# Optimization experiments

Hardware: AMD Instinct MI355X
Metric: run time of the kernel (lower is better)

The kernel has to match this reference:

```python
import math
import jax, jax.numpy as jnp
import numpy as np

BSZ, SEQ, DIM = 2, 2048, 4096
N_HEADS, N_KV = 32, 8
HEAD_DIM = DIM // N_HEADS  # 128
N_REP = N_HEADS // N_KV    # 4
EPS = 1e-5
ROPE_THETA = 500000.0


def setup_inputs() -> dict:
    key = jax.random.key(0)
    ks = jax.random.split(key, 6)
    scale = 0.02
    x = jax.random.normal(ks[0], (BSZ, SEQ, DIM), dtype=jnp.float32)
    wq = jax.random.normal(ks[1], (N_HEADS * HEAD_DIM, DIM), dtype=jnp.float32) * scale
    wk = jax.random.normal(ks[2], (N_KV * HEAD_DIM, DIM), dtype=jnp.float32) * scale
    wv = jax.random.normal(ks[3], (N_KV * HEAD_DIM, DIM), dtype=jnp.float32) * scale
    wo = jax.random.normal(ks[4], (N_HEADS * HEAD_DIM, DIM), dtype=jnp.float32).T * scale  # [DIM, n_heads*hd] -> stored as [out,in]
    wo = jax.random.normal(ks[4], (DIM, N_HEADS * HEAD_DIM), dtype=jnp.float32) * scale
    # RoPE tables (real/imag parts of freqs_cis)
    inv_freq = 1.0 / (ROPE_THETA ** (jnp.arange(0, HEAD_DIM, 2, dtype=jnp.float32) / HEAD_DIM))
    angles = jnp.arange(SEQ, dtype=jnp.float32)[:, None] * inv_freq[None, :]  # [SEQ, HEAD_DIM//2]
    cos, sin = jnp.cos(angles), jnp.sin(angles)
    # causal additive mask
    neg_inf = jnp.finfo(jnp.float32).min
    mask = jnp.where(jnp.tril(jnp.ones((SEQ, SEQ), dtype=bool)), 0.0, neg_inf).astype(jnp.float32)
    return {"x": x, "wq": wq, "wk": wk, "wv": wv, "wo": wo,
            "cos": cos, "sin": sin, "mask": mask, "start_pos": 0}


def _apply_rope(t, cos, sin):
    # t: [b, s, h, hd]; pairs (even, odd) as in view_as_complex
    tf = t.astype(jnp.float32).reshape(*t.shape[:-1], HEAD_DIM // 2, 2)
    e, o = tf[..., 0], tf[..., 1]
    c = cos[None, :, None, :]
    s = sin[None, :, None, :]
    out = jnp.stack([e * c - o * s, e * s + o * c], axis=-1)
    return out.reshape(t.shape).astype(t.dtype)


def _rmsnorm(t):
    tf = t.astype(jnp.float32)
    return (tf * jax.lax.rsqrt(jnp.mean(tf * tf, axis=-1, keepdims=True) + EPS)).astype(t.dtype)


def reference(x, wq, wk, wv, wo, cos, sin, mask, start_pos):
    b, s, _ = x.shape
    xq = (x @ wq.T).reshape(b, s, N_HEADS, HEAD_DIM)
    xk = (x @ wk.T).reshape(b, s, N_KV, HEAD_DIM)
    xv = (x @ wv.T).reshape(b, s, N_KV, HEAD_DIM)
    xq = _apply_rope(xq, cos, sin)
    xk = _apply_rope(xk, cos, sin)
    xq = _rmsnorm(xq)
    xk = _rmsnorm(xk)
    # KV cache write/read with start_pos=0 over seqlen tokens is identity here.
    # GQA without repeat_interleave: q head h attends kv head h // N_REP
    q = xq.transpose(0, 2, 1, 3).reshape(b, N_KV, N_REP, s, HEAD_DIM)
    k = xk.transpose(0, 2, 1, 3)  # [b, n_kv, s, hd]
    v = xv.transpose(0, 2, 1, 3)
    scale = 1.0 / math.sqrt(HEAD_DIM)
    scores = jnp.einsum('bgrqd,bgkd->bgrqk', q, k) * scale + mask[None, None, None]
    probs = jax.nn.softmax(scores, axis=-1)
    out = jnp.einsum('bgrqk,bgkd->bgrqd', probs, v)
    out = out.reshape(b, N_HEADS, s, HEAD_DIM).transpose(0, 2, 1, 3).reshape(b, s, N_HEADS * HEAD_DIM)
    return out @ wo.T
```

## Files before the change

kernel.cpp:

```cpp
#include <hip/hip_runtime.h>
#include <hip/hip_bf16.h>
#include <stdint.h>

#define SEQ 2048
#define DIMSZ 4096
#define QKVN 6144

typedef __attribute__((ext_vector_type(8))) __bf16 bf16x8;
typedef __attribute__((ext_vector_type(4))) float f32x4;

static __device__ __forceinline__ void gld_lds16(const void* g, void* l) {
  __builtin_amdgcn_global_load_lds(
      (__attribute__((address_space(1))) void*)(g),
      (__attribute__((address_space(3))) void*)(l), 16, 0, 0);
}

__global__ __launch_bounds__(256) void k_cvt5(const float* __restrict__ x,
                                              const float* __restrict__ wq,
                                              const float* __restrict__ wk,
                                              const float* __restrict__ wv,
                                              const float* __restrict__ wo,
                                              __bf16* __restrict__ xb,
                                              __bf16* __restrict__ wqkvb,
                                              __bf16* __restrict__ wob) {
  long vid = (long)blockIdx.x * 256 + threadIdx.x;
  const long stride = (long)gridDim.x * 256;
  for (; vid < 7340032L; vid += stride) {
    const float* src; __bf16* dst; long off;
    if (vid < 2097152L)      { src = x;  dst = xb;                off = vid; }
    else if (vid < 4194304L) { src = wq; dst = wqkvb;             off = vid - 2097152L; }
    else if (vid < 4718592L) { src = wk; dst = wqkvb + 16777216L; off = vid - 4194304L; }
    else if (vid < 5242880L) { src = wv; dst = wqkvb + 20971520L; off = vid - 4718592L; }
    else                     { src = wo; dst = wob;               off = vid - 5242880L; }
    const long e = off * 8;
    float4 v0 = *(const float4*)(src + e);
    float4 v1 = *(const float4*)(src + e + 4);
    bf16x8 o;
    o[0] = (__bf16)v0.x; o[1] = (__bf16)v0.y; o[2] = (__bf16)v0.z; o[3] = (__bf16)v0.w;
    o[4] = (__bf16)v1.x; o[5] = (__bf16)v1.y; o[6] = (__bf16)v1.z; o[7] = (__bf16)v1.w;
    *(bf16x8*)(dst + e) = o;
  }
}

template <typename OutT>
__global__ __launch_bounds__(512) void k_gemm8p(const __bf16* __restrict__ A,
                                                const __bf16* __restrict__ B,
                                                OutT* __restrict__ C,
                                                int M, int N, int K) {
  __shared__ __align__(16) __bf16 As[2][2][128 * 64];
  __shared__ __align__(16) __bf16 Bs[2][2][128 * 64];
  const int t = threadIdx.x;
  const int l = t & 63;
  const int w = t >> 6;
  const int wm = w >> 2;
  const int wn = w & 3;
  const int lr = l & 15, lg = l >> 4;
  const int sw = lr & 7;
  const int bm = blockIdx.y, bn = blockIdx.x;

  const int srow = t >> 3;
  const int scol = ((t & 7) ^ (srow & 7)) << 3;
  const __bf16* pa0 = A + (size_t)(bm * 256 +   0 + srow) * K + scol;
  const __bf16* pa1 = A + (size_t)(bm * 256 +  64 + srow) * K + scol;
  const __bf16* pa2 = A + (size_t)(bm * 256 + 128 + srow) * K + scol;
  const __bf16* pa3 = A + (size_t)(bm * 256 + 192 + srow) * K + scol;
  const __bf16* pb0 = B + (size_t)(bn * 256 +   0 + srow) * K + scol;
  const __bf16* pb1 = B + (size_t)(bn * 256 +  64 + srow) * K + scol;
  const __bf16* pb2 = B + (size_t)(bn * 256 + 128 + srow) * K + scol;
  const __bf16* pb3 = B + (size_t)(bn * 256 + 192 + srow) * K + scol;
  const int ldst = t * 8;

#define SA0(buf, kc) { gld_lds16(pa0 + (kc), &As[buf][0][ldst]); gld_lds16(pa1 + (kc), &As[buf][0][4096 + ldst]); }
#define SA1(buf, kc) { gld_lds16(pa2 + (kc), &As[buf][1][ldst]); gld_lds16(pa3 + (kc), &As[buf][1][4096 + ldst]); }
#define SB0(buf, kc) { gld_lds16(pb0 + (kc), &Bs[buf][0][ldst]); gld_lds16(pb1 + (kc), &Bs[buf][0][4096 + ldst]); }
#define SB1(buf, kc) { gld_lds16(pb2 + (kc), &Bs[buf][1][ldst]); gld_lds16(pb3 + (kc), &Bs[buf][1][4096 + ldst]); }

  const int c0 = ((lg ^ sw) * 8);
  const int c1 = (((lg ^ sw) ^ 4) * 8);
  const int aRow = lr;
  const int bRow = (wn & 1) * 64 + lr;

#define RDA(mi0, cur)                                                          \
  _Pragma("unroll") for (int mi = 0; mi < 4; ++mi) {                           \
    a[mi][0] = *(const bf16x8*)&As[cur][wm][(((mi0) + mi) * 16 + aRow) * 64 + c0]; \
    a[mi][1] = *(const bf16x8*)&As[cur][wm][(((mi0) + mi) * 16 + aRow) * 64 + c1]; \
  }
#define RDB(bv, ni0, cur)                                                      \
  _Pragma("unroll") for (int ni = 0; ni < 2; ++ni) {                           \
    bv[ni][0] = *(const bf16x8*)&Bs[cur][wn >> 1][(((ni0) + ni) * 16 + bRow) * 64 + c0]; \
    bv[ni][1] = *(const bf16x8*)&Bs[cur][wn >> 1][(((ni0) + ni) * 16 + bRow) * 64 + c1]; \
  }
#define PHTOP()                                        \
  asm volatile("" ::: "memory");                       \
  __builtin_amdgcn_s_barrier();                        \
  asm volatile("s_waitcnt lgkmcnt(0)" ::: "memory");   \
  __builtin_amdgcn_s_setprio(1)
#define PHEND()                                        \
  __builtin_amdgcn_s_setprio(0);                       \
  asm volatile("" ::: "memory");                       \
  __builtin_amdgcn_s_barrier()
#define PHENDW()                                       \
  __builtin_amdgcn_s_setprio(0);                       \
  asm volatile("s_waitcnt vmcnt(4)" ::: "memory");     \
  __builtin_amdgcn_s_barrier()
#define MMA16(am0, bv, ni0)                                                    \
  _Pragma("unroll") for (int mi = 0; mi < 4; ++mi)                             \
  _Pragma("unroll") for (int ni = 0; ni < 2; ++ni)                             \
  _Pragma("unroll") for (int kk = 0; kk < 2; ++kk)                             \
    acc[(am0) + mi][(ni0) + ni] = __builtin_amdgcn_mfma_f32_16x16x32_bf16(     \
        a[mi][kk], bv[ni][kk], acc[(am0) + mi][(ni0) + ni], 0, 0, 0);

  f32x4 acc[8][4] = {};
  const int nt = K >> 6;
  const int niter = nt >> 1;

  SB0(0, 0); SA0(0, 0); SA1(0, 0); SB1(0, 0);
  SB0(1, 64); SA0(1, 64);
  asm volatile("s_waitcnt vmcnt(4)" ::: "memory");
  asm volatile("" ::: "memory");
  __builtin_amdgcn_s_barrier();
  asm volatile("" ::: "memory");

  for (int i = 0; i < niter; ++i) {
    const int kT1 = (2 * i + 1) << 6;
    const int k2  = (2 * i + 2 < nt ? 2 * i + 2 : nt - 1) << 6;
    const int k3  = (2 * i + 3 < nt ? 2 * i + 3 : nt - 1) << 6;
    bf16x8 a[4][2], b0[2][2], b1[2][2];

    RDA(0, 0); RDB(b0, 0, 0);
    SA1(1, kT1);
    PHTOP(); MMA16(0, b0, 0); PHEND();
    RDB(b1, 2, 0);
    SB1(1, kT1);
    PHTOP(); MMA16(0, b1, 2); PHEND();
    RDA(4, 0);
    SB0(0, k2);
    PHTOP(); MMA16(4, b1, 2); PHEND();
    SA0(0, k2);
    PHTOP(); MMA16(4, b0, 0); PHENDW();

    RDA(0, 1); RDB(b0, 0, 1);
    SA1(0, k2);
    PHTOP(); MMA16(0, b0, 0); PHEND();
    RDB(b1, 2, 1);
    SB1(0, k2);
    PHTOP(); MMA16(0, b1, 2); PHEND();
    RDA(4, 1);
    SB0(1, k3);
    PHTOP(); MMA16(4, b1, 2); PHEND();
    SA0(1, k3);
    PHTOP(); MMA16(4, b0, 0); PHENDW();
  }
#undef SA0
#undef SA1
#undef SB0
#undef SB1
#undef RDA
#undef RDB
#undef PHTOP
#undef PHEND
#undef PHENDW
#undef MMA16

  const int row0 = bm * 256 + wm * 128;
  const int col0 = bn * 256 + wn * 64;
#pragma unroll
  for (int mi = 0; mi < 8; ++mi)
#pragma unroll
    for (int ni = 0; ni < 4; ++ni)
#pragma unroll
      for (int r = 0; r < 4; ++r)
        C[(size_t)(row0 + mi * 16 + lg * 4 + r) * N + (col0 + ni * 16 + lr)] =
            (OutT)acc[mi][ni][r];
}

__global__ __launch_bounds__(256) void k_rope_norm(__bf16* __restrict__ qkv,
                                                   const float* __restrict__ cosT,
                                                   const float* __restrict__ sinT) {
  const int task = blockIdx.x * 4 + (threadIdx.x >> 6);
  const int l = threadIdx.x & 63;
  const int m = task / 40;
  const int h = task - m * 40;
  const int s = m & (SEQ - 1);
  const bool isQ = h < 32;
  const int col = isQ ? h * 128 : 4096 + (h - 32) * 128;
  __bf16* p = qkv + (size_t)m * QKVN + col + l * 2;
  float e = (float)p[0], o = (float)p[1];
  float c = cosT[s * 64 + l], sn = sinT[s * 64 + l];
  float e2 = e * c - o * sn;
  float o2 = e * sn + o * c;
  float ss = e2 * e2 + o2 * o2;
#pragma unroll
  for (int off = 32; off > 0; off >>= 1) ss += __shfl_xor(ss, off);
  float r = rsqrtf(ss * (1.0f / 128.0f) + 1e-5f);
  if (isQ) r *= 0.08838834764831845f;
  p[0] = (__bf16)(e2 * r);
  p[1] = (__bf16)(o2 * r);
}

__global__ __launch_bounds__(256) void k_transpose_v(const __bf16* __restrict__ qkv,
                                                     __bf16* __restrict__ vt) {
  __shared__ __bf16 tile[64][136];
  const int t = threadIdx.x;
  const int st = blockIdx.x, bg = blockIdx.y;
  const int b = bg >> 3, g = bg & 7;
  const int s0 = st * 64;
#pragma unroll
  for (int p = 0; p < 4; ++p) {
    int row = p * 16 + (t >> 4);
    int co = (t & 15) * 8;
    *(bf16x8*)&tile[row][co] =
        *(const bf16x8*)&qkv[(size_t)(b * SEQ + s0 + row) * QKVN + 5120 + g * 128 + co];
  }
  __syncthreads();
#pragma unroll
  for (int p = 0; p < 4; ++p) {
    int d = p * 32 + (t >> 3);
    int so = (t & 7) * 8;
    bf16x8 v;
#pragma unroll
    for (int j = 0; j < 8; ++j) v[j] = tile[so + j][d];
    *(bf16x8*)&vt[((size_t)bg * 128 + d) * SEQ + s0 + so] = v;
  }
}

__global__ __launch_bounds__(256) void k_flash(const __bf16* __restrict__ qkv,
                                               const __bf16* __restrict__ vt,
                                               __bf16* __restrict__ attno) {
  __shared__ __bf16 Ks[64 * 128];
  __shared__ __bf16 Vs[128 * 64];
  __shared__ __bf16 Ps[4][16 * 64];
  const int t = threadIdx.x, w = t >> 6, l = t & 63;
  const int lr = l & 15, lg = l >> 4;
  const int bh = blockIdx.y;
  const int b = bh >> 5, h = bh & 31, g = h >> 2;
  const int qt0 = blockIdx.x, qt1 = 31 - (int)blockIdx.x;

  const __bf16* kp = qkv + 4096 + (size_t)(b * SEQ + (t >> 4)) * QKVN + g * 128 +
                     (((t & 15) ^ ((t >> 4) & 7)) * 8);
  const __bf16* vp = vt + (size_t)(b * 8 + g) * 128 * SEQ + (size_t)(t >> 3) * SEQ +
                     (((t & 7) ^ ((t >> 3) & 7)) * 8);
  const int wbase = (t & ~63) * 8;
  const int sw = lr & 7;

  for (int pass = 0; pass < 2; ++pass) {
    const int qt = (pass == 0) ? qt0 : qt1;

    const __bf16* Qb = qkv + (size_t)(b * SEQ + qt * 64 + w * 16 + lr) * QKVN + h * 128;
    bf16x8 qf[4];
#pragma unroll
    for (int kk = 0; kk < 4; ++kk) qf[kk] = *(const bf16x8*)&Qb[kk * 32 + lg * 8];

    f32x4 oacc[8] = {};
    float mrow[4], lsum[4];
#pragma unroll
    for (int r = 0; r < 4; ++r) { mrow[r] = -1e30f; lsum[r] = 0.f; }

    for (int kt = 0; kt <= qt; ++kt) {
      const size_t kv0 = (size_t)kt * 64;
#pragma unroll
      for (int i = 0; i < 4; ++i)
        gld_lds16(kp + (kv0 + i * 16) * QKVN, &Ks[i * 2048 + wbase]);
#pragma unroll
      for (int i = 0; i < 4; ++i)
        gld_lds16(vp + (size_t)i * 32 * SEQ + kv0, &Vs[i * 2048 + wbase]);
      __syncthreads();

      f32x4 sc[4] = {};
      __builtin_amdgcn_s_setprio(1);
#pragma unroll
      for (int kk = 0; kk < 4; ++kk)
#pragma unroll
        for (int n = 0; n < 4; ++n) {
          bf16x8 kf = *(const bf16x8*)&Ks[(n * 16 + lr) * 128 + ((kk * 4 + lg) ^ sw) * 8];
          sc[n] = __builtin_amdgcn_mfma_f32_16x16x32_bf16(qf[kk], kf, sc[n], 0, 0, 0);
        }
      __builtin_amdgcn_s_setprio(0);

      if (kt == qt) {
#pragma unroll
        for (int n = 0; n < 4; ++n)
#pragma unroll
          for (int r = 0; r < 4; ++r)
            if (n * 16 + lr > w * 16 + lg * 4 + r) sc[n][r] = -1e30f;
      }

      float pml[4];
      float need = -1e30f;
#pragma unroll
      for (int r = 0; r < 4; ++r) {
        pml[r] = fmaxf(fmaxf(sc[0][r], sc[1][r]), fmaxf(sc[2][r], sc[3][r]));
        need = fmaxf(need, pml[r] - mrow[r]);
      }
      if (__all(need <= 8.0f)) {
#pragma unroll
        for (int r = 0; r < 4; ++r) {
          float ps = 0.f;
#pragma unroll
          for (int n = 0; n < 4; ++n) { sc[n][r] = __expf(sc[n][r] - mrow[r]); ps += sc[n][r]; }
#pragma unroll
          for (int off = 8; off > 0; off >>= 1) ps += __shfl_xor(ps, off);
          lsum[r] += ps;
        }
      } else {
#pragma unroll
        for (int r = 0; r < 4; ++r) {
          float pm = pml[r];
#pragma unroll
          for (int off = 8; off > 0; off >>= 1) pm = fmaxf(pm, __shfl_xor(pm, off));
          float mn = fmaxf(mrow[r], pm);
          float corr = __expf(mrow[r] - mn);
          mrow[r] = mn;
          float ps = 0.f;
#pragma unroll
          for (int n = 0; n < 4; ++n) { sc[n][r] = __expf(sc[n][r] - mn); ps += sc[n][r]; }
#pragma unroll
          for (int off = 8; off > 0; off >>= 1) ps += __shfl_xor(ps, off);
          lsum[r] = lsum[r] * corr + ps;
#pragma unroll
          for (int dn = 0; dn < 8; ++dn) oacc[dn][r] *= corr;
        }
      }

#pragma unroll
      for (int n = 0; n < 4; ++n)
#pragma unroll
        for (int r = 0; r < 4; ++r) {
          int row = lg * 4 + r;
          Ps[w][row * 64 + (((n * 2 + (lr >> 3)) ^ (row & 7)) * 8) + (lr & 7)] = (__bf16)sc[n][r];
        }

      __builtin_amdgcn_s_setprio(1);
#pragma unroll
      for (int ks = 0; ks < 2; ++ks) {
        bf16x8 pf = *(const bf16x8*)&Ps[w][lr * 64 + ((ks * 4 + lg) ^ sw) * 8];
#pragma unroll
        for (int dn = 0; dn < 8; ++dn) {
          bf16x8 vf = *(const bf16x8*)&Vs[(dn * 16 + lr) * 64 + ((ks * 4 + lg) ^ sw) * 8];
          oacc[dn] = __builtin_amdgcn_mfma_f32_16x16x32_bf16(pf, vf, oacc[dn], 0, 0, 0);
        }
      }
      __builtin_amdgcn_s_setprio(0);
      __syncthreads();
    }

    float inv[4];
#pragma unroll
    for (int r = 0; r < 4; ++r) inv[r] = __builtin_amdgcn_rcpf(lsum[r]);
    __bf16* Ob = attno + (size_t)(b * SEQ + qt * 64 + w * 16) * DIMSZ + h * 128;
#pragma unroll
    for (int dn = 0; dn < 8; ++dn)
#pragma unroll
      for (int r = 0; r < 4; ++r)
        Ob[(size_t)(lg * 4 + r) * DIMSZ + dn * 16 + lr] = (__bf16)(oacc[dn][r] * inv[r]);
  }
}

extern "C" void kernel_launch(void* const* d_in, const int* in_sizes, int n_in,
                              void* d_out, int out_size, void* d_ws, size_t ws_size,
                              hipStream_t stream) {
  const float* x    = (const float*)d_in[0];
  const float* wq   = (const float*)d_in[1];
  const float* wk   = (const float*)d_in[2];
  const float* wv   = (const float*)d_in[3];
  const float* wo   = (const float*)d_in[4];
  const float* cosT = (const float*)d_in[5];
  const float* sinT = (const float*)d_in[6];

  char* ws = (char*)d_ws;
  __bf16* xb    = (__bf16*)(ws);
  __bf16* wqkvb = (__bf16*)(ws + 33554432);
  __bf16* qkvb  = (__bf16*)(ws + 83886080);
  __bf16* wob   = (__bf16*)(ws + 134217728);
  __bf16* vt    = (__bf16*)(ws + 167772160);
  __bf16* attno = (__bf16*)(ws + 176160768);
  float* out = (float*)d_out;

  k_cvt5<<<4096, 256, 0, stream>>>(x, wq, wk, wv, wo, xb, wqkvb, wob);

  k_gemm8p<__bf16><<<dim3(24, 16), 512, 0, stream>>>(xb, wqkvb, qkvb, 4096, QKVN, 4096);
  k_rope_norm<<<40960, 256, 0, stream>>>(qkvb, cosT, sinT);
  k_transpose_v<<<dim3(32, 16), 256, 0, stream>>>(qkvb, vt);
  k_flash<<<dim3(16, 64), 256, 0, stream>>>(qkvb, vt, attno);
  k_gemm8p<float><<<dim3(16, 16), 512, 0, stream>>>(attno, wob, out, 4096, DIMSZ, 4096);
}
```

Measured before the change: 597.9 us.

## Double-buffer K/V tiles in flash attention with async LDS prefetch

Splits the K and V shared-memory tiles into two buffers and issues the global-to-LDS loads for the next key tile before computing on the current one. Manual vmcnt waits and raw barriers let the prefetch stay in flight during the QK and PV MFMA work. The aim is to hide global load latency behind compute. In exchange, LDS use roughly doubles, which may lower occupancy, and the hand-written waitcnt counts depend on the load instruction count staying exact.

```diff
diff --git a/kernel.cpp b/kernel.cpp
--- a/kernel.cpp
+++ b/kernel.cpp
@@ -227,8 +227,8 @@
 __global__ __launch_bounds__(256) void k_flash(const __bf16* __restrict__ qkv,
                                                const __bf16* __restrict__ vt,
                                                __bf16* __restrict__ attno) {
-  __shared__ __bf16 Ks[64 * 128];
-  __shared__ __bf16 Vs[128 * 64];
+  __shared__ __bf16 Ks[2][64 * 128];
+  __shared__ __bf16 Vs[2][128 * 64];
   __shared__ __bf16 Ps[4][16 * 64];
   const int t = threadIdx.x, w = t >> 6, l = t & 63;
   const int lr = l & 15, lg = l >> 4;
@@ -243,6 +243,14 @@
   const int wbase = (t & ~63) * 8;
   const int sw = lr & 7;
 
+#define STAGE_KV(buf, kv)                                                    \
+  do {                                                                       \
+    _Pragma("unroll") for (int i_ = 0; i_ < 4; ++i_)                         \
+        gld_lds16(kp + ((kv) + i_ * 16) * QKVN, &Ks[buf][i_ * 2048 + wbase]);\
+    _Pragma("unroll") for (int i_ = 0; i_ < 4; ++i_)                         \
+        gld_lds16(vp + (size_t)(i_ * 32) * SEQ + (kv), &Vs[buf][i_ * 2048 + wbase]); \
+  } while (0)
+
   for (int pass = 0; pass < 2; ++pass) {
     const int qt = (pass == 0) ? qt0 : qt1;
 
@@ -256,15 +264,19 @@
 #pragma unroll
     for (int r = 0; r < 4; ++r) { mrow[r] = -1e30f; lsum[r] = 0.f; }
 
+    STAGE_KV(0, (size_t)0);
+
     for (int kt = 0; kt <= qt; ++kt) {
-      const size_t kv0 = (size_t)kt * 64;
-#pragma unroll
-      for (int i = 0; i < 4; ++i)
-        gld_lds16(kp + (kv0 + i * 16) * QKVN, &Ks[i * 2048 + wbase]);
-#pragma unroll
-      for (int i = 0; i < 4; ++i)
-        gld_lds16(vp + (size_t)i * 32 * SEQ + kv0, &Vs[i * 2048 + wbase]);
-      __syncthreads();
+      const int buf = kt & 1;
+      if (kt < qt) {
+        STAGE_KV(buf ^ 1, (size_t)(kt + 1) * 64);
+        asm volatile("s_waitcnt vmcnt(8)" ::: "memory");
+      } else {
+        asm volatile("s_waitcnt vmcnt(0)" ::: "memory");
+      }
+      asm volatile("" ::: "memory");
+      __builtin_amdgcn_s_barrier();
+      asm volatile("" ::: "memory");
 
       f32x4 sc[4] = {};
       __builtin_amdgcn_s_setprio(1);
@@ -272,7 +284,7 @@
       for (int kk = 0; kk < 4; ++kk)
 #pragma unroll
         for (int n = 0; n < 4; ++n) {
-          bf16x8 kf = *(const bf16x8*)&Ks[(n * 16 + lr) * 128 + ((kk * 4 + lg) ^ sw) * 8];
+          bf16x8 kf = *(const bf16x8*)&Ks[buf][(n * 16 + lr) * 128 + ((kk * 4 + lg) ^ sw) * 8];
           sc[n] = __builtin_amdgcn_mfma_f32_16x16x32_bf16(qf[kk], kf, sc[n], 0, 0, 0);
         }
       __builtin_amdgcn_s_setprio(0);
@@ -336,12 +348,14 @@
         bf16x8 pf = *(const bf16x8*)&Ps[w][lr * 64 + ((ks * 4 + lg) ^ sw) * 8];
 #pragma unroll
         for (int dn = 0; dn < 8; ++dn) {
-          bf16x8 vf = *(const bf16x8*)&Vs[(dn * 16 + lr) * 64 + ((ks * 4 + lg) ^ sw) * 8];
+          bf16x8 vf = *(const bf16x8*)&Vs[buf][(dn * 16 + lr) * 64 + ((ks * 4 + lg) ^ sw) * 8];
           oacc[dn] = __builtin_amdgcn_mfma_f32_16x16x32_bf16(pf, vf, oacc[dn], 0, 0, 0);
         }
       }
       __builtin_amdgcn_s_setprio(0);
-      __syncthreads();
+      asm volatile("" ::: "memory");
+      __builtin_amdgcn_s_barrier();
+      asm volatile("" ::: "memory");
     }
 
     float inv[4];
@@ -354,6 +368,7 @@
       for (int r = 0; r < 4; ++r)
         Ob[(size_t)(lg * 4 + r) * DIMSZ + dn * 16 + lr] = (__bf16)(oacc[dn][r] * inv[r]);
   }
+#undef STAGE_KV
 }
 
 extern "C" void kernel_launch(void* const* d_in, const int* in_sizes, int n_in,
```

New measurement: 697.9 us. +16.7%, slower.
